# Performance work log

Measured on AMD Instinct MI355X. Metric: run time of the kernel, lower is better.

Reference implementation:

```python
import jax, jax.numpy as jnp
import numpy as np

# dims
V, D, H = 30000, 300, 300
NS, L = 10000, 32
B, NMAX, MMAX = 256, 128, 128
EPS = 0.1          # sinkhorn entropic regularizer
ITERS = 50         # fixed sinkhorn sweeps (replaces convergence check, jit-friendly)
NEG = 1e9
PAD = 0


def setup_inputs() -> dict:
    key = jax.random.key(0)
    ks = jax.random.split(key, 12)
    data = jax.random.randint(ks[0], (NS, L), 0, V, dtype=jnp.int32)
    row_idx = jax.random.randint(ks[1], (B, NMAX), 0, NS, dtype=jnp.int32)
    col_idx = jax.random.randint(ks[2], (B, MMAX), 0, NS, dtype=jnp.int32)
    row_len = jax.random.randint(ks[3], (B,), 1, NMAX + 1, dtype=jnp.int32)
    col_len = jax.random.randint(ks[4], (B,), 1, MMAX + 1, dtype=jnp.int32)
    g = lambda k, shape, fan: (jax.random.normal(k, shape, jnp.float32) / np.sqrt(fan)).astype(jnp.float32)
    return {
        'data': data, 'row_idx': row_idx, 'col_idx': col_idx,
        'row_len': row_len, 'col_len': col_len,
        'emb': g(ks[5], (V, D), D),
        'W1': g(ks[6], (D, H), D), 'b1': jnp.zeros((H,), jnp.float32),
        'W2': g(ks[7], (H, H), H), 'b2': jnp.zeros((H,), jnp.float32),
        'Wc': g(ks[8], (2 * H, H), 2 * H), 'bc': jnp.zeros((H,), jnp.float32),
        'Wcls': g(ks[9], (2 * H, H), 2 * H), 'bcls': jnp.zeros((H,), jnp.float32),
        'Wout': g(ks[10], (H, 2), H), 'bout': jnp.zeros((2,), jnp.float32),
    }


def _forward(data, row_idx, col_idx, row_len, col_len,
             emb, W1, b1, W2, b2, Wc, bc, Wcls, bcls, Wout, bout):
    # ---- Embedder: token embedding + masked mean pool over tokens ----
    tok = emb[data]                                        # [NS, L, D]
    tmask = (data != PAD).astype(tok.dtype)[..., None]     # [NS, L, 1]
    enc = (tok * tmask).sum(1) / jnp.clip(tmask.sum(1), 1.0)   # [NS, D]
    # ---- attention_forward: 2-layer FFN ----
    henc = jax.nn.relu(jax.nn.relu(enc @ W1 + b1) @ W2 + b2)   # [NS, H]
    # ---- variable-length gather + pad (scope) ----
    rows = henc[row_idx]                                   # [B, NMAX, H]
    cols = henc[col_idx]                                   # [B, MMAX, H]
    rmask = (jnp.arange(NMAX)[None, :] < row_len[:, None]).astype(henc.dtype)
    cmask = (jnp.arange(MMAX)[None, :] < col_len[:, None]).astype(henc.dtype)
    rows = rows * rmask[..., None]
    cols = cols * cmask[..., None]
    # ---- batched pairwise cosine cost ----
    rn = rows / (jnp.linalg.norm(rows, axis=-1, keepdims=True) + 1e-8)
    cn = cols / (jnp.linalg.norm(cols, axis=-1, keepdims=True) + 1e-8)
    C = 1.0 - jnp.einsum('bnd,bmd->bnm', rn, cn)           # [B, NMAX, MMAX]
    pmask = rmask[:, :, None] * cmask[:, None, :]
    Cm = jnp.where(pmask > 0, C, 1e4)
    # uniform marginals over valid rows/cols (log-domain, -inf -> -NEG on pads)
    loga = jnp.where(rmask > 0, -jnp.log(row_len.astype(C.dtype))[:, None], -NEG)
    logb = jnp.where(cmask > 0, -jnp.log(col_len.astype(C.dtype))[:, None], -NEG)
    # ---- log-domain Sinkhorn (row/col marginal rescaling) ----
    def step(carry, _):
        f, g = carry
        f = EPS * loga - EPS * jax.nn.logsumexp((g[:, None, :] - Cm) / EPS, axis=2)
        g = EPS * logb - EPS * jax.nn.logsumexp((f[:, :, None] - Cm) / EPS, axis=1)
        return (f, g), None
    (f, g), _ = jax.lax.scan(step, (jnp.zeros_like(loga), jnp.zeros_like(logb)), None, length=ITERS)
    P = jnp.exp((f[:, :, None] + g[:, None, :] - Cm) / EPS) * pmask  # [B, NMAX, MMAX]
    # ---- attend: column_alignments @ rows, row_alignments @ columns ----
    attended_row = jnp.einsum('bnm,bnd->bmd', P, rows)     # P^T @ rows
    attended_col = jnp.einsum('bnm,bmd->bnd', P, cols)     # P @ cols
    # ---- compare_forward (1 layer) + masked sum ----
    cr = jax.nn.relu(jnp.concatenate([rows, attended_col], -1) @ Wc + bc)
    cr = (cr * rmask[..., None]).sum(1)                    # [B, H]
    cc = jax.nn.relu(jnp.concatenate([cols, attended_row], -1) @ Wc + bc)
    cc = (cc * cmask[..., None]).sum(1)                    # [B, H]
    # ---- cls_forward + out ----
    z = jax.nn.relu(jnp.concatenate([cr, cc], -1) @ Wcls + bcls)
    return z @ Wout + bout                                 # [B, 2]


def reference(data, row_idx, col_idx, row_len, col_len,
              emb, W1, b1, W2, b2, Wc, bc, Wcls, bcls, Wout, bout):
    return _forward(data, row_idx, col_idx, row_len, col_len,
                    emb, W1, b1, W2, b2, Wc, bc, Wcls, bcls, Wout, bout)
```

## Files before the change

kernel.cpp:

```cpp
#include <hip/hip_runtime.h>
#include <math.h>

#define NS 10000
#define LSEQ 32
#define DDIM 300
#define HDIM 300
#define BB 256
#define NMAX 128
#define MMAX 128
#define EPSR 0.1f
#define SITERS 50
#define KPAD 320
#define NPADW 384

typedef __attribute__((ext_vector_type(8))) short bf16x8;
typedef __attribute__((ext_vector_type(4))) float f32x4;

__device__ __forceinline__ ushort f2bf(float x) {
  union { float f; unsigned u; } c; c.f = x;
  unsigned r = (c.u + 0x7fffu + ((c.u >> 16) & 1u)) >> 16;
  return (ushort)r;
}
__device__ __forceinline__ float bf2f(ushort h) {
  union { unsigned u; float f; } c; c.u = ((unsigned)h) << 16;
  return c.f;
}

__global__ __launch_bounds__(256) void k_embed(const int* __restrict__ data,
                                               const float* __restrict__ emb,
                                               ushort* __restrict__ enchi,
                                               ushort* __restrict__ enclo) {
  __shared__ int ids[LSEQ];
  __shared__ __align__(16) float4 part[3][76];
  int s = blockIdx.x;
  int tid = threadIdx.x;
  if (tid < LSEQ) ids[tid] = data[s * LSEQ + tid];
  __syncthreads();
  int cnt = 0;
#pragma unroll
  for (int t = 0; t < LSEQ; ++t) cnt += (ids[t] != 0) ? 1 : 0;
  int g = tid / 75, d = tid - g * 75;
  const float4* emb4 = (const float4*)emb;
  if (g < 3) {
    float4 acc = make_float4(0.f, 0.f, 0.f, 0.f);
    for (int t = g; t < LSEQ; t += 3) {
      int id = ids[t];
      if (id != 0) {
        float4 e = emb4[(size_t)id * 75 + d];
        acc.x += e.x; acc.y += e.y; acc.z += e.z; acc.w += e.w;
      }
    }
    part[g][d] = acc;
  }
  __syncthreads();
  if (g == 0) {
    float4 a = part[0][d], b = part[1][d], c = part[2][d];
    float inv = 1.f / (float)(cnt > 0 ? cnt : 1);
    float v[4] = {(a.x + b.x + c.x) * inv, (a.y + b.y + c.y) * inv,
                  (a.z + b.z + c.z) * inv, (a.w + b.w + c.w) * inv};
    ushort4 h, l;
    h.x = f2bf(v[0]); l.x = f2bf(v[0] - bf2f(h.x));
    h.y = f2bf(v[1]); l.y = f2bf(v[1] - bf2f(h.y));
    h.z = f2bf(v[2]); l.z = f2bf(v[2] - bf2f(h.z));
    h.w = f2bf(v[3]); l.w = f2bf(v[3] - bf2f(h.w));
    *(ushort4*)&enchi[(size_t)s * KPAD + d * 4] = h;
    *(ushort4*)&enclo[(size_t)s * KPAD + d * 4] = l;
  } else if (g == 1 && d < 5) {
    ushort4 z; z.x = z.y = z.z = z.w = 0;
    *(ushort4*)&enchi[(size_t)s * KPAD + 300 + d * 4] = z;
    *(ushort4*)&enclo[(size_t)s * KPAD + 300 + d * 4] = z;
  }
}

__global__ __launch_bounds__(256) void k_cvt_all(
    const float* __restrict__ W1, const float* __restrict__ W2,
    const float* __restrict__ Wc, ushort* __restrict__ W1hi,
    ushort* __restrict__ W1lo, ushort* __restrict__ W2hi,
    ushort* __restrict__ W2lo, ushort* __restrict__ Wchi,
    ushort* __restrict__ Wclo) {
  int i = blockIdx.x * 256 + threadIdx.x;
  const int SA = NPADW * KPAD;
  const int SC = 640 * KPAD;
  float v = 0.f;
  ushort *ph, *pl;
  int idx;
  if (i < SA) {
    idx = i;
    int n = idx / KPAD, k = idx - n * KPAD;
    if (n < HDIM && k < DDIM) v = W1[(size_t)k * HDIM + n];
    ph = W1hi; pl = W1lo;
  } else if (i < 2 * SA) {
    idx = i - SA;
    int n = idx / KPAD, k = idx - n * KPAD;
    if (n < HDIM && k < HDIM) v = W2[(size_t)k * HDIM + n];
    ph = W2hi; pl = W2lo;
  } else if (i < 2 * SA + SC) {
    idx = i - 2 * SA;
    int n = idx / KPAD, k = idx - n * KPAD;
    if (k < HDIM && n < 2 * HDIM)
      v = (n < HDIM) ? Wc[(size_t)k * HDIM + n]
                     : Wc[(size_t)(HDIM + k) * HDIM + (n - HDIM)];
    ph = Wchi; pl = Wclo;
  } else {
    return;
  }
  ushort h = f2bf(v);
  ph[idx] = h;
  pl[idx] = f2bf(v - bf2f(h));
}

__global__ __launch_bounds__(256) void k_gemm_mfma(
    const ushort* __restrict__ Ahi, const ushort* __restrict__ Alo,
    const ushort* __restrict__ BhiT, const ushort* __restrict__ BloT,
    const float* __restrict__ bias, int M, int N, int relu,
    float* __restrict__ Cf, ushort* __restrict__ Chi,
    ushort* __restrict__ Clo) {
  __shared__ __align__(16) ushort ldsA[2][64][40];
  __shared__ __align__(16) ushort ldsB[2][128][40];
  int tid = threadIdx.x;
  int m0 = blockIdx.x * 64, n0 = blockIdx.y * 128;
  int rowA = tid >> 2, chA = (tid & 3) * 8;
  int rowB = tid >> 1, chB = (tid & 1) * 16;
  bool mok = (m0 + rowA) < M;
  const ushort* pAh = Ahi + (size_t)(m0 + rowA) * KPAD + chA;
  const ushort* pAl = Alo + (size_t)(m0 + rowA) * KPAD + chA;
  const ushort* pBh = BhiT + (size_t)(n0 + rowB) * KPAD + chB;
  const ushort* pBl = BloT + (size_t)(n0 + rowB) * KPAD + chB;
  uint4 rAh, rAl, rBh0, rBh1, rBl0, rBl1;
  uint4 z4; z4.x = z4.y = z4.z = z4.w = 0;
  auto ld = [&](int c) {
    int o = c * 32;
    rAh = mok ? *(const uint4*)(pAh + o) : z4;
    rAl = mok ? *(const uint4*)(pAl + o) : z4;
    rBh0 = *(const uint4*)(pBh + o);
    rBh1 = *(const uint4*)(pBh + o + 8);
    rBl0 = *(const uint4*)(pBl + o);
    rBl1 = *(const uint4*)(pBl + o + 8);
  };
  auto st = [&]() {
    *(uint4*)&ldsA[0][rowA][chA] = rAh;
    *(uint4*)&ldsA[1][rowA][chA] = rAl;
    *(uint4*)&ldsB[0][rowB][chB] = rBh0;
    *(uint4*)&ldsB[0][rowB][chB + 8] = rBh1;
    *(uint4*)&ldsB[1][rowB][chB] = rBl0;
    *(uint4*)&ldsB[1][rowB][chB + 8] = rBl1;
  };
  int w = tid >> 6, lane = tid & 63;
  int q = lane >> 4, l16 = lane & 15;
  int mh = w >> 1, nh = w & 1;
  f32x4 zf = {0.f, 0.f, 0.f, 0.f};
  f32x4 acc[2][4];
#pragma unroll
  for (int s = 0; s < 2; ++s)
#pragma unroll
    for (int t = 0; t < 4; ++t) acc[s][t] = zf;
  ld(0); st(); __syncthreads();
  for (int c = 0; c < 10; ++c) {
    if (c < 9) ld(c + 1);
    bf16x8 ah0 = *(const bf16x8*)&ldsA[0][mh * 32 + l16][q * 8];
    bf16x8 ah1 = *(const bf16x8*)&ldsA[0][mh * 32 + 16 + l16][q * 8];
    bf16x8 al0 = *(const bf16x8*)&ldsA[1][mh * 32 + l16][q * 8];
    bf16x8 al1 = *(const bf16x8*)&ldsA[1][mh * 32 + 16 + l16][q * 8];
#pragma unroll
    for (int t = 0; t < 4; ++t) {
      int brow = nh * 64 + t * 16 + l16;
      bf16x8 bh = *(const bf16x8*)&ldsB[0][brow][q * 8];
      bf16x8 bl = *(const bf16x8*)&ldsB[1][brow][q * 8];
      acc[0][t] = __builtin_amdgcn_mfma_f32_16x16x32_bf16(ah0, bh, acc[0][t], 0, 0, 0);
      acc[0][t] = __builtin_amdgcn_mfma_f32_16x16x32_bf16(ah0, bl, acc[0][t], 0, 0, 0);
      acc[0][t] = __builtin_amdgcn_mfma_f32_16x16x32_bf16(al0, bh, acc[0][t], 0, 0, 0);
      acc[1][t] = __builtin_amdgcn_mfma_f32_16x16x32_bf16(ah1, bh, acc[1][t], 0, 0, 0);
      acc[1][t] = __builtin_amdgcn_mfma_f32_16x16x32_bf16(ah1, bl, acc[1][t], 0, 0, 0);
      acc[1][t] = __builtin_amdgcn_mfma_f32_16x16x32_bf16(al1, bh, acc[1][t], 0, 0, 0);
    }
    __syncthreads();
    if (c < 9) st();
    __syncthreads();
  }
#pragma unroll
  for (int t = 0; t < 4; ++t) {
    int n = n0 + nh * 64 + t * 16 + l16;
    bool nin = n < N;
    float bz = (bias && nin) ? bias[n] : 0.f;
#pragma unroll
    for (int s = 0; s < 2; ++s) {
#pragma unroll
      for (int r = 0; r < 4; ++r) {
        int m = m0 + mh * 32 + s * 16 + q * 4 + r;
        if (m >= M) continue;
        float v = acc[s][t][r] + bz;
        if (relu) v = v > 0.f ? v : 0.f;
        if (Cf && nin) Cf[(size_t)m * N + n] = v;
        if (Chi && n < KPAD) {
          ushort h = 0, l = 0;
          if (nin) { h = f2bf(v); l = f2bf(v - bf2f(h)); }
          Chi[(size_t)m * KPAD + n] = h;
          Clo[(size_t)m * KPAD + n] = l;
        }
      }
    }
  }
}

__global__ __launch_bounds__(256) void k_norm_split(
    const ushort* __restrict__ hehi, const ushort* __restrict__ helo,
    ushort* __restrict__ hnhi, ushort* __restrict__ hnlo) {
  int s = blockIdx.x * 4 + (threadIdx.x >> 6);
  int lane = threadIdx.x & 63;
  if (s >= NS) return;
  const ushort* ph = hehi + (size_t)s * KPAD;
  const ushort* pl = helo + (size_t)s * KPAD;
  float x[5];
  float ss = 0.f;
#pragma unroll
  for (int q = 0; q < 5; ++q) {
    int d = lane + q * 64;
    x[q] = bf2f(ph[d]) + bf2f(pl[d]);
    ss += x[q] * x[q];
  }
#pragma unroll
  for (int off = 32; off > 0; off >>= 1) ss += __shfl_down(ss, off, 64);
  ss = __shfl(ss, 0, 64);
  float inv = 1.f / (sqrtf(ss) + 1e-8f);
  ushort* qh = hnhi + (size_t)s * KPAD;
  ushort* ql = hnlo + (size_t)s * KPAD;
#pragma unroll
  for (int q = 0; q < 5; ++q) {
    int d = lane + q * 64;
    float v = x[q] * inv;
    ushort h = f2bf(v);
    qh[d] = h;
    ql[d] = f2bf(v - bf2f(h));
  }
}

__global__ __launch_bounds__(256) void k_cost_mfma(
    const ushort* __restrict__ hnhi, const ushort* __restrict__ hnlo,
    const int* __restrict__ ridx, const int* __restrict__ cidx,
    const int* __restrict__ rlen, const int* __restrict__ clen,
    float* __restrict__ Kmat) {
  int b = blockIdx.z;
  int r0 = blockIdx.x * 64, c0 = blockIdx.y * 64;
  int rl = rlen[b], cl = clen[b];
  float* Kg = Kmat + (size_t)b * NMAX * MMAX;
  int tid = threadIdx.x;
  if (r0 >= rl || c0 >= cl) {
    for (int l = tid; l < 64 * 16; l += 256) {
      int i = l >> 4, j = (l & 15) << 2;
      *(float4*)&Kg[(size_t)(r0 + i) * MMAX + c0 + j] =
          make_float4(0.f, 0.f, 0.f, 0.f);
    }
    return;
  }
  __shared__ int rix[64], cix[64];
  __shared__ __align__(16) ushort lds[4][64][40];
  if (tid < 64) rix[tid] = ridx[b * NMAX + r0 + tid];
  else if (tid < 128) cix[tid - 64] = cidx[b * MMAX + c0 + tid - 64];
  __syncthreads();
  int row = tid >> 2, ch = tid & 3;
  const ushort* pRh = hnhi + (size_t)rix[row] * KPAD + ch * 8;
  const ushort* pRl = hnlo + (size_t)rix[row] * KPAD + ch * 8;
  const ushort* pCh = hnhi + (size_t)cix[row] * KPAD + ch * 8;
  const ushort* pCl = hnlo + (size_t)cix[row] * KPAD + ch * 8;
  uint4 rRh, rRl, rCh, rCl;
  auto ld = [&](int c) {
    int o = c * 32;
    rRh = *(const uint4*)(pRh + o);
    rRl = *(const uint4*)(pRl + o);
    rCh = *(const uint4*)(pCh + o);
    rCl = *(const uint4*)(pCl + o);
  };
  auto st = [&]() {
    *(uint4*)&lds[0][row][ch * 8] = rRh;
    *(uint4*)&lds[1][row][ch * 8] = rRl;
    *(uint4*)&lds[2][row][ch * 8] = rCh;
    *(uint4*)&lds[3][row][ch * 8] = rCl;
  };
  int w = tid >> 6, lane = tid & 63;
  int q = lane >> 4, l16 = lane & 15;
  int mh = w >> 1, nh = w & 1;
  f32x4 zf = {0.f, 0.f, 0.f, 0.f};
  f32x4 acc[2][2];
#pragma unroll
  for (int s = 0; s < 2; ++s)
#pragma unroll
    for (int t = 0; t < 2; ++t) acc[s][t] = zf;
  ld(0); st(); __syncthreads();
  for (int c = 0; c < 10; ++c) {
    if (c < 9) ld(c + 1);
    bf16x8 ah0 = *(const bf16x8*)&lds[0][mh * 32 + l16][q * 8];
    bf16x8 ah1 = *(const bf16x8*)&lds[0][mh * 32 + 16 + l16][q * 8];
    bf16x8 al0 = *(const bf16x8*)&lds[1][mh * 32 + l16][q * 8];
    bf16x8 al1 = *(const bf16x8*)&lds[1][mh * 32 + 16 + l16][q * 8];
#pragma unroll
    for (int t = 0; t < 2; ++t) {
      int brow = nh * 32 + t * 16 + l16;
      bf16x8 bh = *(const bf16x8*)&lds[2][brow][q * 8];
      bf16x8 bl = *(const bf16x8*)&lds[3][brow][q * 8];
      acc[0][t] = __builtin_amdgcn_mfma_f32_16x16x32_bf16(ah0, bh, acc[0][t], 0, 0, 0);
      acc[0][t] = __builtin_amdgcn_mfma_f32_16x16x32_bf16(ah0, bl, acc[0][t], 0, 0, 0);
      acc[0][t] = __builtin_amdgcn_mfma_f32_16x16x32_bf16(al0, bh, acc[0][t], 0, 0, 0);
      acc[1][t] = __builtin_amdgcn_mfma_f32_16x16x32_bf16(ah1, bh, acc[1][t], 0, 0, 0);
      acc[1][t] = __builtin_amdgcn_mfma_f32_16x16x32_bf16(ah1, bl, acc[1][t], 0, 0, 0);
      acc[1][t] = __builtin_amdgcn_mfma_f32_16x16x32_bf16(al1, bh, acc[1][t], 0, 0, 0);
    }
    __syncthreads();
    if (c < 9) st();
    __syncthreads();
  }
#pragma unroll
  for (int t = 0; t < 2; ++t) {
    int n = c0 + nh * 32 + t * 16 + l16;
#pragma unroll
    for (int s = 0; s < 2; ++s) {
#pragma unroll
      for (int r = 0; r < 4; ++r) {
        int m = r0 + mh * 32 + s * 16 + q * 4 + r;
        float kv = (m < rl && n < cl) ? expf((acc[s][t][r] - 1.f) / EPSR) : 0.f;
        Kg[(size_t)m * MMAX + n] = kv;
      }
    }
  }
}

__global__ __launch_bounds__(512) void k_sinkhorn(
    float* __restrict__ Kmat, const int* __restrict__ rlen,
    const int* __restrict__ clen) {
  __shared__ __align__(16) float vq[4][36];
  __shared__ __align__(16) float uq[4][36];
  int b = blockIdx.x;
  int tid = threadIdx.x;
  int n = tid >> 2, q = tid & 3;
  int rl = rlen[b], cl = clen[b];
  float* Kg = Kmat + (size_t)b * NMAX * MMAX;
  float kr[32], kt[32];
  const float4* Kg4 = (const float4*)(Kg + (size_t)n * MMAX + 32 * q);
#pragma unroll
  for (int t = 0; t < 8; ++t) *(float4*)&kr[4 * t] = Kg4[t];
#pragma unroll
  for (int j = 0; j < 32; ++j) kt[j] = Kg[(size_t)(32 * q + j) * MMAX + n];
  if (tid < 128) vq[tid >> 5][tid & 31] = (tid < cl) ? 1.f : 0.f;
  float av = (n < rl) ? 1.f / (float)rl : 0.f;
  float bv = (n < cl) ? 1.f / (float)cl : 0.f;
  float un = 0.f;
  __syncthreads();
  for (int it = 0; it < SITERS; ++it) {
    float s = 0.f;
#pragma unroll
    for (int t = 0; t < 8; ++t) {
      float4 vv = *(const float4*)&vq[q][4 * t];
      s += kr[4 * t + 0] * vv.x + kr[4 * t + 1] * vv.y +
           kr[4 * t + 2] * vv.z + kr[4 * t + 3] * vv.w;
    }
    s += __shfl_xor(s, 1, 64);
    s += __shfl_xor(s, 2, 64);
    un = (n < rl) ? av / s : 0.f;
    if (q == 0) uq[n >> 5][n & 31] = un;
    __syncthreads();
    float s2 = 0.f;
#pragma unroll
    for (int t = 0; t < 8; ++t) {
      float4 uu = *(const float4*)&uq[q][4 * t];
      s2 += kt[4 * t + 0] * uu.x + kt[4 * t + 1] * uu.y +
            kt[4 * t + 2] * uu.z + kt[4 * t + 3] * uu.w;
    }
    s2 += __shfl_xor(s2, 1, 64);
    s2 += __shfl_xor(s2, 2, 64);
    float vm = (n < cl) ? bv / s2 : 0.f;
    if (q == 0) vq[n >> 5][n & 31] = vm;
    __syncthreads();
  }
  float4* Pg4 = (float4*)(Kg + (size_t)n * MMAX + 32 * q);
#pragma unroll
  for (int t = 0; t < 8; ++t) {
    float4 vv = *(const float4*)&vq[q][4 * t];
    float4 p;
    p.x = un * kr[4 * t + 0] * vv.x;
    p.y = un * kr[4 * t + 1] * vv.y;
    p.z = un * kr[4 * t + 2] * vv.z;
    p.w = un * kr[4 * t + 3] * vv.w;
    Pg4[t] = p;
  }
}

__global__ __launch_bounds__(256) void k_att_cmp_both(
    const float* __restrict__ P, const float* __restrict__ HcB,
    const int* __restrict__ row_idx, const int* __restrict__ col_idx,
    const int* __restrict__ row_len, const int* __restrict__ col_len,
    const float* __restrict__ bc, float* __restrict__ cr,
    float* __restrict__ cc) {
  int b = blockIdx.y;
  int side = blockIdx.z;
  int c0 = blockIdx.x * 64;
  const int* idx_main = side == 0 ? row_idx : col_idx;
  const int* idx_other = side == 0 ? col_idx : row_idx;
  int lm = side == 0 ? row_len[b] : col_len[b];
  int lo = side == 0 ? col_len[b] : row_len[b];
  float* outacc = side == 0 ? cr : cc;
  __shared__ __align__(16) float smem[2][2][16][68];
  __shared__ int iox[NMAX];
  __shared__ int imx[NMAX];
  int tid = threadIdx.x, tx = tid & 15, ty = tid >> 4;
  int jj = tid & 63, kq = tid >> 6;
  if (tid < 128) iox[tid] = idx_other[b * NMAX + tid];
  else imx[tid - 128] = idx_main[b * NMAX + tid - 128];
  __syncthreads();
  const float* Pb = P + (size_t)b * NMAX * MMAX;
  bool cok = (c0 + jj) < HDIM;
  int nkc = (lo + 15) >> 4;
  int nmt = (lm + 63) >> 6;
  float pR[4], gR[4];
  auto loadPG = [&](int mt, int kc) {
    int m0 = mt * 64, k0 = kc * 16;
    if (side == 0) {
#pragma unroll
      for (int p = 0; p < 4; ++p)
        pR[p] = Pb[(size_t)(m0 + ty + p * 16) * MMAX + k0 + tx];
    } else {
#pragma unroll
      for (int p = 0; p < 4; ++p)
        pR[p] = Pb[(size_t)(k0 + kq + p * 4) * MMAX + m0 + jj];
    }
#pragma unroll
    for (int p = 0; p < 4; ++p) {
      int row = iox[k0 + kq + p * 4];
      gR[p] = cok ? HcB[(size_t)row * 600 + 300 + c0 + jj] : 0.f;
    }
  };
  auto storePG = [&](int buf) {
    if (side == 0) {
#pragma unroll
      for (int p = 0; p < 4; ++p) smem[buf][0][tx][ty + p * 16] = pR[p];
    } else {
#pragma unroll
      for (int p = 0; p < 4; ++p) smem[buf][0][kq + p * 4][jj] = pR[p];
    }
#pragma unroll
    for (int p = 0; p < 4; ++p) smem[buf][1][kq + p * 4][jj] = gR[p];
  };
  float colsum[4] = {0.f, 0.f, 0.f, 0.f};
  loadPG(0, 0);
  storePG(0);
  __syncthreads();
  int cur = 0;
  for (int mt = 0; mt < nmt; ++mt) {
    float acc[4][4] = {};
    for (int kc = 0; kc < nkc; ++kc) {
      bool last = (mt == nmt - 1) && (kc == nkc - 1);
      if (!last) {
        int nm = (kc + 1 < nkc) ? mt : mt + 1;
        int nk = (kc + 1 < nkc) ? kc + 1 : 0;
        loadPG(nm, nk);
      }
#pragma unroll
      for (int kk = 0; kk < 16; ++kk) {
        float4 av = *(const float4*)&smem[cur][0][kk][ty * 4];
        float4 gv = *(const float4*)&smem[cur][1][kk][tx * 4];
        float a[4] = {av.x, av.y, av.z, av.w};
        float g[4] = {gv.x, gv.y, gv.z, gv.w};
#pragma unroll
        for (int i = 0; i < 4; ++i)
#pragma unroll
          for (int j = 0; j < 4; ++j) acc[i][j] += a[i] * g[j];
      }
      if (!last) storePG(cur ^ 1);
      __syncthreads();
      cur ^= 1;
    }
#pragma unroll
    for (int i = 0; i < 4; ++i) {
      int mi = mt * 64 + ty * 4 + i;
      if (mi >= lm) continue;
      int hrow = imx[mi];
#pragma unroll
      for (int j = 0; j < 4; ++j) {
        int col = c0 + tx * 4 + j;
        if (col >= HDIM) continue;
        float y = acc[i][j] + HcB[(size_t)hrow * 600 + col] + bc[col];
        colsum[j] += y > 0.f ? y : 0.f;
      }
    }
  }
  __syncthreads();
  float(*red)[68] = (float(*)[68]) & smem[0][0][0][0];
#pragma unroll
  for (int j = 0; j < 4; ++j) red[ty][tx * 4 + j] = colsum[j];
  __syncthreads();
  if (tid < 64) {
    float s = 0.f;
#pragma unroll
    for (int r = 0; r < 16; ++r) s += red[r][tid];
    int col = c0 + tid;
    if (col < HDIM) outacc[(size_t)b * HDIM + col] = s;
  }
}

__global__ __launch_bounds__(320) void k_cls(
    const float* __restrict__ cr, const float* __restrict__ cc,
    const float* __restrict__ Wcls, const float* __restrict__ bcls,
    const float* __restrict__ Wout, const float* __restrict__ bout,
    float* __restrict__ out) {
  __shared__ __align__(16) float cz[2 * HDIM];
  __shared__ float zz[HDIM];
  int b = blockIdx.x, tid = threadIdx.x;
  if (tid < HDIM) {
    cz[tid] = cr[(size_t)b * HDIM + tid];
    cz[HDIM + tid] = cc[(size_t)b * HDIM + tid];
  }
  __syncthreads();
  if (tid < HDIM) {
    float acc = bcls[tid];
    for (int k4 = 0; k4 < 2 * HDIM; k4 += 4) {
      float4 c = *(const float4*)&cz[k4];
      acc += c.x * Wcls[(size_t)(k4 + 0) * HDIM + tid] +
             c.y * Wcls[(size_t)(k4 + 1) * HDIM + tid] +
             c.z * Wcls[(size_t)(k4 + 2) * HDIM + tid] +
             c.w * Wcls[(size_t)(k4 + 3) * HDIM + tid];
    }
    zz[tid] = acc > 0.f ? acc : 0.f;
  }
  __syncthreads();
  int o = tid >> 6, lane = tid & 63;
  if (o < 2) {
    float p = 0.f;
    for (int j = lane; j < HDIM; j += 64) p += zz[j] * Wout[(size_t)j * 2 + o];
#pragma unroll
    for (int off = 32; off > 0; off >>= 1) p += __shfl_down(p, off, 64);
    if (lane == 0) out[b * 2 + o] = p + bout[o];
  }
}

extern "C" void kernel_launch(void* const* d_in, const int* in_sizes, int n_in,
                              void* d_out, int out_size, void* d_ws, size_t ws_size,
                              hipStream_t stream) {
  (void)in_sizes; (void)n_in; (void)out_size; (void)ws_size;
  const int* data = (const int*)d_in[0];
  const int* row_idx = (const int*)d_in[1];
  const int* col_idx = (const int*)d_in[2];
  const int* row_len = (const int*)d_in[3];
  const int* col_len = (const int*)d_in[4];
  const float* emb = (const float*)d_in[5];
  const float* W1 = (const float*)d_in[6];
  const float* b1 = (const float*)d_in[7];
  const float* W2 = (const float*)d_in[8];
  const float* b2 = (const float*)d_in[9];
  const float* Wc = (const float*)d_in[10];
  const float* bc = (const float*)d_in[11];
  const float* Wcls = (const float*)d_in[12];
  const float* bcls = (const float*)d_in[13];
  const float* Wout = (const float*)d_in[14];
  const float* bout = (const float*)d_in[15];
  float* out = (float*)d_out;

  char* wp = (char*)d_ws;
  auto carve = [&](size_t bytes) {
    char* p = wp; wp += (bytes + 255) & ~(size_t)255; return p;
  };
  ushort* enchi = (ushort*)carve((size_t)NS * KPAD * 2);
  ushort* enclo = (ushort*)carve((size_t)NS * KPAD * 2);
  ushort* h1hi = (ushort*)carve((size_t)NS * KPAD * 2);
  ushort* h1lo = (ushort*)carve((size_t)NS * KPAD * 2);
  ushort* hehi = (ushort*)carve((size_t)NS * KPAD * 2);
  ushort* helo = (ushort*)carve((size_t)NS * KPAD * 2);
  ushort* hnhi = (ushort*)carve((size_t)NS * KPAD * 2);
  ushort* hnlo = (ushort*)carve((size_t)NS * KPAD * 2);
  ushort* W1hi = (ushort*)carve((size_t)NPADW * KPAD * 2);
  ushort* W1lo = (ushort*)carve((size_t)NPADW * KPAD * 2);
  ushort* W2hi = (ushort*)carve((size_t)NPADW * KPAD * 2);
  ushort* W2lo = (ushort*)carve((size_t)NPADW * KPAD * 2);
  ushort* Wchi = (ushort*)carve((size_t)640 * KPAD * 2);
  ushort* Wclo = (ushort*)carve((size_t)640 * KPAD * 2);
  float* HcB = (float*)carve((size_t)NS * 600 * 4);
  float* Km = (float*)carve((size_t)BB * NMAX * MMAX * 4);
  float* cr = (float*)carve((size_t)BB * HDIM * 4);
  float* cc = (float*)carve((size_t)BB * HDIM * 4);

  int gM = (NS + 63) / 64;
  int cvtTotal = 2 * NPADW * KPAD + 640 * KPAD;

  k_embed<<<NS, 256, 0, stream>>>(data, emb, enchi, enclo);
  k_cvt_all<<<(cvtTotal + 255) / 256, 256, 0, stream>>>(
      W1, W2, Wc, W1hi, W1lo, W2hi, W2lo, Wchi, Wclo);
  k_gemm_mfma<<<dim3(gM, 3), 256, 0, stream>>>(
      enchi, enclo, W1hi, W1lo, b1, NS, HDIM, 1, nullptr, h1hi, h1lo);
  k_gemm_mfma<<<dim3(gM, 3), 256, 0, stream>>>(
      h1hi, h1lo, W2hi, W2lo, b2, NS, HDIM, 1, nullptr, hehi, helo);
  k_norm_split<<<(NS + 3) / 4, 256, 0, stream>>>(hehi, helo, hnhi, hnlo);
  k_gemm_mfma<<<dim3(gM, 5), 256, 0, stream>>>(
      hehi, helo, Wchi, Wclo, nullptr, NS, 2 * HDIM, 0, HcB, nullptr, nullptr);
  k_cost_mfma<<<dim3(2, 2, BB), 256, 0, stream>>>(hnhi, hnlo, row_idx, col_idx,
                                                  row_len, col_len, Km);
  k_sinkhorn<<<BB, 512, 0, stream>>>(Km, row_len, col_len);
  k_att_cmp_both<<<dim3(5, BB, 2), 256, 0, stream>>>(
      Km, HcB, row_idx, col_idx, row_len, col_len, bc, cr, cc);
  k_cls<<<BB, 320, 0, stream>>>(cr, cc, Wcls, bcls, Wout, bout, out);
}
```

Measured before the change: 405.7 us.

## Preload whole P tile and gathered columns into registers in compare kernel

Restructures the compare kernel's loads. All gathered other-side HcB values for every k-chunk are loaded into registers once per block, and all P values for a 64-row m-tile are prefetched in one batch instead of one 16-wide chunk at a time. The main-side HcB values and bias are also held in registers, with float4 loads for the main side. This is meant to raise memory-level parallelism and cut per-chunk global load latency, at the cost of many more registers (about 64 extra floats) and possibly lower occupancy.

```diff
diff --git a/kernel.cpp b/kernel.cpp
--- a/kernel.cpp
+++ b/kernel.cpp
@@ -409,79 +409,101 @@
   bool cok = (c0 + jj) < HDIM;
   int nkc = (lo + 15) >> 4;
   int nmt = (lm + 63) >> 6;
-  float pR[4], gR[4];
-  auto loadPG = [&](int mt, int kc) {
-    int m0 = mt * 64, k0 = kc * 16;
-    if (side == 0) {
-#pragma unroll
-      for (int p = 0; p < 4; ++p)
-        pR[p] = Pb[(size_t)(m0 + ty + p * 16) * MMAX + k0 + tx];
-    } else {
-#pragma unroll
-      for (int p = 0; p < 4; ++p)
-        pR[p] = Pb[(size_t)(k0 + kq + p * 4) * MMAX + m0 + jj];
-    }
-#pragma unroll
-    for (int p = 0; p < 4; ++p) {
-      int row = iox[k0 + kq + p * 4];
-      gR[p] = cok ? HcB[(size_t)row * 600 + 300 + c0 + jj] : 0.f;
+  float bb[4];
+#pragma unroll
+  for (int j = 0; j < 4; ++j) {
+    int col = c0 + tx * 4 + j;
+    bb[j] = (col < HDIM) ? bc[col] : 0.f;
+  }
+  float gReg[8][4];
+#pragma unroll
+  for (int kc = 0; kc < 8; ++kc) {
+    if (kc < nkc) {
+#pragma unroll
+      for (int p = 0; p < 4; ++p) {
+        int row = iox[kc * 16 + kq + p * 4];
+        gReg[kc][p] = cok ? HcB[(size_t)row * 600 + 300 + c0 + jj] : 0.f;
+      }
+    }
+  }
+  float pReg[8][4];
+  float4 m4[4];
+  auto loadP = [&](int mt) {
+    int m0 = mt * 64;
+#pragma unroll
+    for (int kc = 0; kc < 8; ++kc) {
+      if (kc < nkc) {
+        if (side == 0) {
+#pragma unroll
+          for (int p = 0; p < 4; ++p)
+            pReg[kc][p] = Pb[(size_t)(m0 + ty + p * 16) * MMAX + kc * 16 + tx];
+        } else {
+#pragma unroll
+          for (int p = 0; p < 4; ++p)
+            pReg[kc][p] = Pb[(size_t)(kc * 16 + kq + p * 4) * MMAX + m0 + jj];
+        }
+      }
     }
   };
-  auto storePG = [&](int buf) {
-    if (side == 0) {
-#pragma unroll
-      for (int p = 0; p < 4; ++p) smem[buf][0][tx][ty + p * 16] = pR[p];
-    } else {
-#pragma unroll
-      for (int p = 0; p < 4; ++p) smem[buf][0][kq + p * 4][jj] = pR[p];
-    }
-#pragma unroll
-    for (int p = 0; p < 4; ++p) smem[buf][1][kq + p * 4][jj] = gR[p];
+  auto loadMain = [&](int mt) {
+#pragma unroll
+    for (int i = 0; i < 4; ++i) {
+      int mi = mt * 64 + ty * 4 + i;
+      int hrow = imx[mi];
+      m4[i] = *(const float4*)&HcB[(size_t)hrow * 600 + c0 + tx * 4];
+    }
   };
+  loadP(0);
+  loadMain(0);
   float colsum[4] = {0.f, 0.f, 0.f, 0.f};
-  loadPG(0, 0);
-  storePG(0);
-  __syncthreads();
-  int cur = 0;
   for (int mt = 0; mt < nmt; ++mt) {
     float acc[4][4] = {};
-    for (int kc = 0; kc < nkc; ++kc) {
-      bool last = (mt == nmt - 1) && (kc == nkc - 1);
-      if (!last) {
-        int nm = (kc + 1 < nkc) ? mt : mt + 1;
-        int nk = (kc + 1 < nkc) ? kc + 1 : 0;
-        loadPG(nm, nk);
+#pragma unroll
+    for (int kc = 0; kc < 8; ++kc) {
+      if (kc < nkc) {
+        int buf = kc & 1;
+        if (side == 0) {
+#pragma unroll
+          for (int p = 0; p < 4; ++p)
+            smem[buf][0][tx][ty + p * 16] = pReg[kc][p];
+        } else {
+#pragma unroll
+          for (int p = 0; p < 4; ++p)
+            smem[buf][0][kq + p * 4][jj] = pReg[kc][p];
+        }
+#pragma unroll
+        for (int p = 0; p < 4; ++p) smem[buf][1][kq + p * 4][jj] = gReg[kc][p];
+        __syncthreads();
+#pragma unroll
+        for (int kk = 0; kk < 16; ++kk) {
+          float4 av = *(const float4*)&smem[buf][0][kk][ty * 4];
+          float4 gv = *(const float4*)&smem[buf][1][kk][tx * 4];
+          float a[4] = {av.x, av.y, av.z, av.w};
+          float g[4] = {gv.x, gv.y, gv.z, gv.w};
+#pragma unroll
+          for (int i = 0; i < 4; ++i)
+#pragma unroll
+            for (int j = 0; j < 4; ++j) acc[i][j] += a[i] * g[j];
+        }
       }
-#pragma unroll
-      for (int kk = 0; kk < 16; ++kk) {
-        float4 av = *(const float4*)&smem[cur][0][kk][ty * 4];
-        float4 gv = *(const float4*)&smem[cur][1][kk][tx * 4];
-        float a[4] = {av.x, av.y, av.z, av.w};
-        float g[4] = {gv.x, gv.y, gv.z, gv.w};
-#pragma unroll
-        for (int i = 0; i < 4; ++i)
-#pragma unroll
-          for (int j = 0; j < 4; ++j) acc[i][j] += a[i] * g[j];
-      }
-      if (!last) storePG(cur ^ 1);
-      __syncthreads();
-      cur ^= 1;
-    }
+    }
+    if (mt + 1 < nmt) loadP(mt + 1);
 #pragma unroll
     for (int i = 0; i < 4; ++i) {
       int mi = mt * 64 + ty * 4 + i;
       if (mi >= lm) continue;
-      int hrow = imx[mi];
 #pragma unroll
       for (int j = 0; j < 4; ++j) {
         int col = c0 + tx * 4 + j;
         if (col >= HDIM) continue;
-        float y = acc[i][j] + HcB[(size_t)hrow * 600 + col] + bc[col];
+        float mv = (&m4[i].x)[j];
+        float y = acc[i][j] + mv + bb[j];
         colsum[j] += y > 0.f ? y : 0.f;
       }
     }
-  }
-  __syncthreads();
+    if (mt + 1 < nmt) loadMain(mt + 1);
+    __syncthreads();
+  }
   float(*red)[68] = (float(*)[68]) & smem[0][0][0][0];
 #pragma unroll
   for (int j = 0; j < 4; ++j) red[ty][tx * 4 + j] = colsum[j];
```

New measurement: 421.9 us. +4.0%, slower.

## Emit split-bf16 P and P^T from Sinkhorn and use MFMA for attention-compare

Applied to the files above, without the earlier changes.

Sinkhorn now writes the transport plan and its transpose as hi/lo bf16 pairs into reused scratch buffers instead of fp32 P. The attention+compare kernel is rewritten to use bf16 MFMA with a three-product split (hi*hi, hi*lo, lo*hi) to keep near-fp32 accuracy. The other-side features are staged once into LDS as split bf16. This replaces the scalar FMA inner loop; it adds extra conversion work and buffer aliasing that overflows into neighbouring scratch regions.

```diff
diff --git a/kernel.cpp b/kernel.cpp
--- a/kernel.cpp
+++ b/kernel.cpp
@@ -325,7 +325,9 @@
 
 __global__ __launch_bounds__(512) void k_sinkhorn(
     float* __restrict__ Kmat, const int* __restrict__ rlen,
-    const int* __restrict__ clen) {
+    const int* __restrict__ clen, ushort* __restrict__ Phi,
+    ushort* __restrict__ Plo, ushort* __restrict__ PThi,
+    ushort* __restrict__ PTlo) {
   __shared__ __align__(16) float vq[4][36];
   __shared__ __align__(16) float uq[4][36];
   int b = blockIdx.x;
@@ -370,25 +372,53 @@
     if (q == 0) vq[n >> 5][n & 31] = vm;
     __syncthreads();
   }
-  float4* Pg4 = (float4*)(Kg + (size_t)n * MMAX + 32 * q);
-#pragma unroll
-  for (int t = 0; t < 8; ++t) {
-    float4 vv = *(const float4*)&vq[q][4 * t];
-    float4 p;
-    p.x = un * kr[4 * t + 0] * vv.x;
-    p.y = un * kr[4 * t + 1] * vv.y;
-    p.z = un * kr[4 * t + 2] * vv.z;
-    p.w = un * kr[4 * t + 3] * vv.w;
-    Pg4[t] = p;
-  }
-}
-
-__global__ __launch_bounds__(256) void k_att_cmp_both(
-    const float* __restrict__ P, const float* __restrict__ HcB,
-    const int* __restrict__ row_idx, const int* __restrict__ col_idx,
-    const int* __restrict__ row_len, const int* __restrict__ col_len,
-    const float* __restrict__ bc, float* __restrict__ cr,
-    float* __restrict__ cc) {
+  float vn = vq[n >> 5][n & 31];
+  size_t rowoff = (size_t)b * (NMAX * MMAX) + (size_t)n * MMAX + 32 * q;
+  {
+    uint hw[16], lw[16];
+#pragma unroll
+    for (int t = 0; t < 16; ++t) {
+      float p0 = un * kr[2 * t] * vq[q][2 * t];
+      float p1 = un * kr[2 * t + 1] * vq[q][2 * t + 1];
+      ushort h0 = f2bf(p0), h1 = f2bf(p1);
+      hw[t] = (uint)h0 | ((uint)h1 << 16);
+      lw[t] = (uint)f2bf(p0 - bf2f(h0)) | ((uint)f2bf(p1 - bf2f(h1)) << 16);
+    }
+#pragma unroll
+    for (int t4 = 0; t4 < 4; ++t4) {
+      uint4 vh = make_uint4(hw[4 * t4], hw[4 * t4 + 1], hw[4 * t4 + 2], hw[4 * t4 + 3]);
+      uint4 vl = make_uint4(lw[4 * t4], lw[4 * t4 + 1], lw[4 * t4 + 2], lw[4 * t4 + 3]);
+      *(uint4*)(Phi + rowoff + 8 * t4) = vh;
+      *(uint4*)(Plo + rowoff + 8 * t4) = vl;
+    }
+  }
+  {
+    uint hw[16], lw[16];
+#pragma unroll
+    for (int t = 0; t < 16; ++t) {
+      float p0 = uq[q][2 * t] * kt[2 * t] * vn;
+      float p1 = uq[q][2 * t + 1] * kt[2 * t + 1] * vn;
+      ushort h0 = f2bf(p0), h1 = f2bf(p1);
+      hw[t] = (uint)h0 | ((uint)h1 << 16);
+      lw[t] = (uint)f2bf(p0 - bf2f(h0)) | ((uint)f2bf(p1 - bf2f(h1)) << 16);
+    }
+#pragma unroll
+    for (int t4 = 0; t4 < 4; ++t4) {
+      uint4 vh = make_uint4(hw[4 * t4], hw[4 * t4 + 1], hw[4 * t4 + 2], hw[4 * t4 + 3]);
+      uint4 vl = make_uint4(lw[4 * t4], lw[4 * t4 + 1], lw[4 * t4 + 2], lw[4 * t4 + 3]);
+      *(uint4*)(PThi + rowoff + 8 * t4) = vh;
+      *(uint4*)(PTlo + rowoff + 8 * t4) = vl;
+    }
+  }
+}
+
+__global__ __launch_bounds__(256) void k_att_mfma(
+    const ushort* __restrict__ Phi, const ushort* __restrict__ Plo,
+    const ushort* __restrict__ PThi, const ushort* __restrict__ PTlo,
+    const float* __restrict__ HcB, const int* __restrict__ row_idx,
+    const int* __restrict__ col_idx, const int* __restrict__ row_len,
+    const int* __restrict__ col_len, const float* __restrict__ bc,
+    float* __restrict__ cr, float* __restrict__ cc) {
   int b = blockIdx.y;
   int side = blockIdx.z;
   int c0 = blockIdx.x * 64;
@@ -396,102 +426,146 @@
   const int* idx_other = side == 0 ? col_idx : row_idx;
   int lm = side == 0 ? row_len[b] : col_len[b];
   int lo = side == 0 ? col_len[b] : row_len[b];
+  const ushort* Ah = (side == 0 ? Phi : PThi) + (size_t)b * (NMAX * MMAX);
+  const ushort* Al = (side == 0 ? Plo : PTlo) + (size_t)b * (NMAX * MMAX);
   float* outacc = side == 0 ? cr : cc;
-  __shared__ __align__(16) float smem[2][2][16][68];
+
+  __shared__ __align__(16) ushort gldh[128][68];
+  __shared__ __align__(16) ushort gldl[128][68];
+  __shared__ float red[4][64];
   __shared__ int iox[NMAX];
   __shared__ int imx[NMAX];
-  int tid = threadIdx.x, tx = tid & 15, ty = tid >> 4;
-  int jj = tid & 63, kq = tid >> 6;
+
+  int tid = threadIdx.x;
+  int w = tid >> 6, lane = tid & 63;
+  int q = lane >> 4, l16 = lane & 15;
   if (tid < 128) iox[tid] = idx_other[b * NMAX + tid];
   else imx[tid - 128] = idx_main[b * NMAX + tid - 128];
   __syncthreads();
-  const float* Pb = P + (size_t)b * NMAX * MMAX;
-  bool cok = (c0 + jj) < HDIM;
-  int nkc = (lo + 15) >> 4;
-  int nmt = (lm + 63) >> 6;
-  float pR[4], gR[4];
-  auto loadPG = [&](int mt, int kc) {
-    int m0 = mt * 64, k0 = kc * 16;
-    if (side == 0) {
-#pragma unroll
-      for (int p = 0; p < 4; ++p)
-        pR[p] = Pb[(size_t)(m0 + ty + p * 16) * MMAX + k0 + tx];
-    } else {
-#pragma unroll
-      for (int p = 0; p < 4; ++p)
-        pR[p] = Pb[(size_t)(k0 + kq + p * 4) * MMAX + m0 + jj];
-    }
-#pragma unroll
-    for (int p = 0; p < 4; ++p) {
-      int row = iox[k0 + kq + p * 4];
-      gR[p] = cok ? HcB[(size_t)row * 600 + 300 + c0 + jj] : 0.f;
-    }
-  };
-  auto storePG = [&](int buf) {
-    if (side == 0) {
-#pragma unroll
-      for (int p = 0; p < 4; ++p) smem[buf][0][tx][ty + p * 16] = pR[p];
-    } else {
-#pragma unroll
-      for (int p = 0; p < 4; ++p) smem[buf][0][kq + p * 4][jj] = pR[p];
-    }
-#pragma unroll
-    for (int p = 0; p < 4; ++p) smem[buf][1][kq + p * 4][jj] = gR[p];
-  };
-  float colsum[4] = {0.f, 0.f, 0.f, 0.f};
-  loadPG(0, 0);
-  storePG(0);
-  __syncthreads();
-  int cur = 0;
-  for (int mt = 0; mt < nmt; ++mt) {
-    float acc[4][4] = {};
-    for (int kc = 0; kc < nkc; ++kc) {
-      bool last = (mt == nmt - 1) && (kc == nkc - 1);
-      if (!last) {
-        int nm = (kc + 1 < nkc) ? mt : mt + 1;
-        int nk = (kc + 1 < nkc) ? kc + 1 : 0;
-        loadPG(nm, nk);
-      }
-#pragma unroll
-      for (int kk = 0; kk < 16; ++kk) {
-        float4 av = *(const float4*)&smem[cur][0][kk][ty * 4];
-        float4 gv = *(const float4*)&smem[cur][1][kk][tx * 4];
-        float a[4] = {av.x, av.y, av.z, av.w};
-        float g[4] = {gv.x, gv.y, gv.z, gv.w};
-#pragma unroll
-        for (int i = 0; i < 4; ++i)
-#pragma unroll
-          for (int j = 0; j < 4; ++j) acc[i][j] += a[i] * g[j];
-      }
-      if (!last) storePG(cur ^ 1);
-      __syncthreads();
-      cur ^= 1;
-    }
-#pragma unroll
-    for (int i = 0; i < 4; ++i) {
-      int mi = mt * 64 + ty * 4 + i;
-      if (mi >= lm) continue;
-      int hrow = imx[mi];
-#pragma unroll
-      for (int j = 0; j < 4; ++j) {
-        int col = c0 + tx * 4 + j;
-        if (col >= HDIM) continue;
-        float y = acc[i][j] + HcB[(size_t)hrow * 600 + col] + bc[col];
-        colsum[j] += y > 0.f ? y : 0.f;
-      }
-    }
-  }
-  __syncthreads();
-  float(*red)[68] = (float(*)[68]) & smem[0][0][0][0];
-#pragma unroll
-  for (int j = 0; j < 4; ++j) red[ty][tx * 4 + j] = colsum[j];
+
+  int nkc = (lo + 31) >> 5;
+  int kmax = nkc * 32;
+  int ndt = (300 - c0 + 15) >> 4;
+  if (ndt > 4) ndt = 4;
+  bool dok = (c0 + lane) < 300;
+
+  {
+    float gv[32];
+#pragma unroll
+    for (int t = 0; t < 32; ++t) {
+      int k = w * 32 + t;
+      gv[t] = (k < lo && dok) ? HcB[(size_t)iox[k] * 600 + 300 + c0 + lane]
+                              : 0.f;
+    }
+#pragma unroll
+    for (int t = 0; t < 32; ++t) {
+      int k = w * 32 + t;
+      if (k < kmax) {
+        ushort h = f2bf(gv[t]);
+        gldh[k][lane] = h;
+        gldl[k][lane] = f2bf(gv[t] - bf2f(h));
+      }
+    }
+  }
+  __syncthreads();
+
+  int i0a = w * 16;
+  int i0b = 64 + w * 16;
+  bool act0 = i0a < lm;
+  bool act1 = i0b < lm;
+  bf16x8 fa0h[4], fa0l[4], fa1h[4], fa1l[4];
+#pragma unroll
+  for (int c = 0; c < 4; ++c) {
+    if (c < nkc) {
+      size_t oa = (size_t)(i0a + l16) * MMAX + 32 * c + 8 * q;
+      size_t ob = (size_t)(i0b + l16) * MMAX + 32 * c + 8 * q;
+      if (act0) {
+        fa0h[c] = *(const bf16x8*)&Ah[oa];
+        fa0l[c] = *(const bf16x8*)&Al[oa];
+      }
+      if (act1) {
+        fa1h[c] = *(const bf16x8*)&Ah[ob];
+        fa1l[c] = *(const bf16x8*)&Al[ob];
+      }
+    }
+  }
+
+  f32x4 zf = {0.f, 0.f, 0.f, 0.f};
+  f32x4 acc0[4], acc1[4];
+#pragma unroll
+  for (int dt = 0; dt < 4; ++dt) { acc0[dt] = zf; acc1[dt] = zf; }
+
+#pragma unroll
+  for (int c = 0; c < 4; ++c) {
+    if (c < nkc) {
+      int kb = 32 * c + 8 * q;
+#pragma unroll
+      for (int dt = 0; dt < 4; ++dt) {
+        if (dt < ndt) {
+          int d = dt * 16 + l16;
+          bf16x8 bh, bl;
+#pragma unroll
+          for (int e = 0; e < 8; ++e) {
+            bh[e] = (short)gldh[kb + e][d];
+            bl[e] = (short)gldl[kb + e][d];
+          }
+          if (act0) {
+            acc0[dt] = __builtin_amdgcn_mfma_f32_16x16x32_bf16(fa0h[c], bh, acc0[dt], 0, 0, 0);
+            acc0[dt] = __builtin_amdgcn_mfma_f32_16x16x32_bf16(fa0h[c], bl, acc0[dt], 0, 0, 0);
+            acc0[dt] = __builtin_amdgcn_mfma_f32_16x16x32_bf16(fa0l[c], bh, acc0[dt], 0, 0, 0);
+          }
+          if (act1) {
+            acc1[dt] = __builtin_amdgcn_mfma_f32_16x16x32_bf16(fa1h[c], bh, acc1[dt], 0, 0, 0);
+            acc1[dt] = __builtin_amdgcn_mfma_f32_16x16x32_bf16(fa1h[c], bl, acc1[dt], 0, 0, 0);
+            acc1[dt] = __builtin_amdgcn_mfma_f32_16x16x32_bf16(fa1l[c], bh, acc1[dt], 0, 0, 0);
+          }
+        }
+      }
+    }
+  }
+
+  float psum[4] = {0.f, 0.f, 0.f, 0.f};
+  float bcv[4];
+#pragma unroll
+  for (int dt = 0; dt < 4; ++dt) {
+    int col = c0 + dt * 16 + l16;
+    bcv[dt] = (col < 300) ? bc[col] : 0.f;
+  }
+#pragma unroll
+  for (int s = 0; s < 2; ++s) {
+    bool act = (s == 0) ? act0 : act1;
+    if (!act) continue;
+    int ibase = ((s == 0) ? i0a : i0b) + q * 4;
+#pragma unroll
+    for (int r = 0; r < 4; ++r) {
+      int i = ibase + r;
+      if (i >= lm) continue;
+      const float* Mrow = &HcB[(size_t)imx[i] * 600];
+#pragma unroll
+      for (int dt = 0; dt < 4; ++dt) {
+        int col = c0 + dt * 16 + l16;
+        if (dt < ndt && col < 300) {
+          float av = (s == 0) ? acc0[dt][r] : acc1[dt][r];
+          float y = av + Mrow[col] + bcv[dt];
+          psum[dt] += y > 0.f ? y : 0.f;
+        }
+      }
+    }
+  }
+#pragma unroll
+  for (int dt = 0; dt < 4; ++dt) {
+    psum[dt] += __shfl_xor(psum[dt], 16, 64);
+    psum[dt] += __shfl_xor(psum[dt], 32, 64);
+  }
+  if (lane < 16) {
+#pragma unroll
+    for (int dt = 0; dt < 4; ++dt) red[w][dt * 16 + lane] = psum[dt];
+  }
   __syncthreads();
   if (tid < 64) {
-    float s = 0.f;
-#pragma unroll
-    for (int r = 0; r < 16; ++r) s += red[r][tid];
+    float s = red[0][tid] + red[1][tid] + red[2][tid] + red[3][tid];
     int col = c0 + tid;
-    if (col < HDIM) outacc[(size_t)b * HDIM + col] = s;
+    if (col < 300) outacc[(size_t)b * HDIM + col] = s;
   }
 }
 
@@ -575,6 +649,11 @@
   float* cr = (float*)carve((size_t)BB * HDIM * 4);
   float* cc = (float*)carve((size_t)BB * HDIM * 4);
 
+  ushort* Phi = enchi;
+  ushort* Plo = h1hi;
+  ushort* PThi = hehi;
+  ushort* PTlo = hnhi;
+
   int gM = (NS + 63) / 64;
   int cvtTotal = 2 * NPADW * KPAD + 640 * KPAD;
 
@@ -590,8 +669,8 @@
       hehi, helo, Wchi, Wclo, nullptr, NS, 2 * HDIM, 0, HcB, nullptr, nullptr);
   k_cost_mfma<<<dim3(2, 2, BB), 256, 0, stream>>>(hnhi, hnlo, row_idx, col_idx,
                                                   row_len, col_len, Km);
-  k_sinkhorn<<<BB, 512, 0, stream>>>(Km, row_len, col_len);
-  k_att_cmp_both<<<dim3(5, BB, 2), 256, 0, stream>>>(
-      Km, HcB, row_idx, col_idx, row_len, col_len, bc, cr, cc);
+  k_sinkhorn<<<BB, 512, 0, stream>>>(Km, row_len, col_len, Phi, Plo, PThi, PTlo);
+  k_att_mfma<<<dim3(5, BB, 2), 256, 0, stream>>>(
+      Phi, Plo, PThi, PTlo, HcB, row_idx, col_idx, row_len, col_len, bc, cr, cc);
   k_cls<<<BB, 320, 0, stream>>>(cr, cc, Wcls, bcls, Wout, bout, out);
 }
```

After: 392.5 us. -3.2%, faster.
